# Performance work log

Hardware: AMD Instinct MI355X
Metric: run time of the kernel (lower is better)

The kernel has to match this reference:

```python
import jax, jax.numpy as jnp
import numpy as np

NEAR, FAR = 2.0, 6.0
N_SAMPLES = 64
L_PTS, L_DIR = 10, 4
INF_DELTA = 1e10


def posenc(x, L):
    # x: [..., 3] -> [..., 3 + 6*L] (identity + sin/cos at 2^l frequencies)
    freqs = 2.0 ** jnp.arange(L, dtype=x.dtype)              # [L]
    ang = x[..., None, :] * freqs[:, None]                   # [..., L, 3]
    enc = jnp.concatenate([jnp.sin(ang), jnp.cos(ang)], axis=-1)  # [..., L, 6]
    return jnp.concatenate([x, enc.reshape(x.shape[:-1] + (L * 6,))], axis=-1)


def setup_inputs() -> dict:
    key = jax.random.key(0)
    ks = jax.random.split(key, 12)
    R, D, DH = 4096, 256, 128
    PE_P, PE_D = 3 + 6 * L_PTS, 3 + 6 * L_DIR  # 63, 27

    def w(k, shape):
        fan_in = shape[0]
        return jax.random.normal(k, shape, dtype=jnp.float32) / np.sqrt(fan_in)

    return {
        "xyz": jax.random.normal(ks[0], (1, R, 3), dtype=jnp.float32),
        "viewdirs": jax.random.normal(ks[1], (1, R, 3), dtype=jnp.float32),
        "W1": w(ks[2], (PE_P, D)), "b1": jnp.zeros((D,), jnp.float32),
        "W2": w(ks[3], (D, D)),    "b2": jnp.zeros((D,), jnp.float32),
        "W3": w(ks[4], (D, D)),    "b3": jnp.zeros((D,), jnp.float32),
        "Wsig": w(ks[5], (D, 1)),  "bsig": jnp.zeros((1,), jnp.float32),
        "Wfeat": w(ks[6], (D, D)), "bfeat": jnp.zeros((D,), jnp.float32),
        "Wdir": w(ks[7], (D + PE_D, DH)), "bdir": jnp.zeros((DH,), jnp.float32),
        "Wrgb": w(ks[8], (DH, 3)), "brgb": jnp.zeros((3,), jnp.float32),
    }


def reference(xyz, viewdirs, W1, b1, W2, b2, W3, b3, Wsig, bsig,
              Wfeat, bfeat, Wdir, bdir, Wrgb, brgb):
    xyz = xyz[0]          # [R, 3] (batch dim squeezed as in render_coarse)
    vd = viewdirs[0]
    vd = vd / jnp.linalg.norm(vd, axis=-1, keepdims=True)
    R = xyz.shape[0]

    # Evenly spaced samples between near and far (perturb=0 -> deterministic)
    t = jnp.linspace(0.0, 1.0, N_SAMPLES, dtype=xyz.dtype)
    samples = NEAR * (1.0 - t) + FAR * t                     # [N]
    samples = jnp.broadcast_to(samples, (R, N_SAMPLES))      # [R, N]
    delta = jnp.concatenate(
        [samples[:, 1:] - samples[:, :-1],
         jnp.full((R, 1), INF_DELTA, dtype=samples.dtype)], axis=-1)  # [R, N]

    # Sample points along each ray
    pts = xyz[:, None, :] + samples[..., None] * vd[:, None, :]  # [R, N, 3]

    # NeRF MLP: positional-encoded points -> density + view-dep color
    pe = posenc(pts, L_PTS)                                   # [R, N, 63]
    de = posenc(vd, L_DIR)                                    # [R, 27]
    h = jax.nn.relu(pe @ W1 + b1)
    h = jax.nn.relu(h @ W2 + b2)
    h = jax.nn.relu(h @ W3 + b3)                              # [R, N, 256]
    density = (h @ Wsig + bsig)[..., 0]                       # [R, N]
    feat = h @ Wfeat + bfeat                                  # [R, N, 256]
    de_b = jnp.broadcast_to(de[:, None, :], (R, N_SAMPLES, de.shape[-1]))
    hd = jax.nn.relu(jnp.concatenate([feat, de_b], axis=-1) @ Wdir + bdir)
    rgb = jax.nn.sigmoid(hd @ Wrgb + brgb)                    # [R, N, 3]

    # Volume rendering (alpha compositing with cumprod transmittance)
    sigma = jax.nn.relu(density)
    alpha = 1.0 - jnp.exp(-sigma * delta)                     # [R, N]
    T = jnp.concatenate(
        [jnp.ones((R, 1), alpha.dtype),
         jnp.cumprod(1.0 - alpha[:, :-1], axis=-1)], axis=-1)
    w = T * alpha                                             # [R, N]
    rgb_map = jnp.sum(w[..., None] * rgb, axis=-2)            # [R, 3]
    alpha_map = jnp.sum(w, axis=-1, keepdims=True)            # [R, 1]
    rgb_map = rgb_map + (1.0 - alpha_map)                     # white_bkgd
    depth_map = jnp.sum(w * samples, axis=-1)                 # [R]
    return rgb_map, depth_map, alpha_map
```

## Files before the change

### kernel.cpp

```cpp
#include <hip/hip_runtime.h>
#include <hip/hip_bf16.h>
#include <math.h>


typedef unsigned short u16;
typedef unsigned int   u32;
typedef __bf16 bf16x8 __attribute__((ext_vector_type(8)));
typedef float  f32x4  __attribute__((ext_vector_type(4)));

#define HI_STRIDE 296
#define LO_STRIDE 264
#define NROW 64

__device__ __align__(16) u16 g_whi[249856];
__device__ __align__(16) u16 g_wlo[147456];

constexpr int OFF_W1 = 0;
constexpr int OFF_W2 = 16384;
constexpr int OFF_W3 = 81920;
constexpr int OFF_WF = 147456;
constexpr int OFF_WD = 212992;

static __device__ __forceinline__ float bf2f(u16 u) {
  return __uint_as_float(((u32)u) << 16);
}
static __device__ __forceinline__ u16 f2bf(float f) {
  u32 x = __float_as_uint(f);
  return (u16)((x + 0x7FFFu + ((x >> 16) & 1u)) >> 16);
}
static __device__ __forceinline__ u32 cvt_pk_bf16(float a, float b) {
  u32 r;
  asm("v_cvt_pk_bf16_f32 %0, %1, %2" : "=v"(r) : "v"(a), "v"(b));
  return r;
}
static __device__ __forceinline__ float wash(float x) {
  return (x == x) ? x : 0.0f;
}

struct alignas(8) U16x4 { u16 x, y, z, w; };

__global__ void repack_kernel(const float* __restrict__ w1, const float* __restrict__ w2,
                              const float* __restrict__ w3, const float* __restrict__ wf,
                              const float* __restrict__ wd) {
  int e = blockIdx.x * 256 + threadIdx.x;
  const float* src; int K, N, ks, base;
  if (e < 81920)       { if (e < 16384) { src = w1; K = 63;  N = 256; ks = 2; base = OFF_W1; }
                         else           { src = w2; K = 256; N = 256; ks = 8; base = OFF_W2; } }
  else if (e < 147456) { src = w3; K = 256; N = 256; ks = 8; base = OFF_W3; }
  else if (e < 212992) { src = wf; K = 256; N = 256; ks = 8; base = OFF_WF; }
  else                 { src = wd; K = 283; N = 128; ks = 9; base = OFF_WD; }
  int le   = e - base;
  int f    = le >> 9, pos = le & 511;
  int lane = pos >> 3, j = pos & 7;
  int t    = f / ks,  s = f - t * ks;
  int k    = s * 32 + ((lane >> 4) << 3) + j;
  int n    = (t << 4) + (lane & 15);
  float v  = (k < K) ? src[k * N + n] : 0.0f;
  u16 h    = f2bf(v);
  g_whi[e] = h;
  if (e < 147456) g_wlo[e] = f2bf(v - bf2f(h));
}

template<int KS, int NT, int RT, bool RELU, bool SPLIT>
static __device__ __forceinline__ void mlp_layer(u16* hi, u16* lo,
                                                 const u16* __restrict__ wh_,
                                                 const u16* __restrict__ wl_,
                                                 const float* __restrict__ bias,
                                                 int rg, int cg, int lane) {
  f32x4 acc[RT][NT];
#pragma unroll
  for (int rt = 0; rt < RT; ++rt)
#pragma unroll
    for (int nt = 0; nt < NT; ++nt) {
      f32x4 z = {0.0f, 0.0f, 0.0f, 0.0f};
      acc[rt][nt] = z;
    }
  const int l15 = lane & 15, q = lane >> 4;
#pragma unroll
  for (int s = 0; s < KS; ++s) {
    bf16x8 ah[RT], al[RT];
#pragma unroll
    for (int rt = 0; rt < RT; ++rt) {
      const int row = (rg * RT + rt) * 16 + l15;
      ah[rt] = *reinterpret_cast<const bf16x8*>(&hi[row * HI_STRIDE + s * 32 + q * 8]);
      if (SPLIT)
        al[rt] = *reinterpret_cast<const bf16x8*>(&lo[row * LO_STRIDE + s * 32 + q * 8]);
    }
    bf16x8 wh[NT], wl[NT];
#pragma unroll
    for (int nt = 0; nt < NT; ++nt) {
      const int t = cg * NT + nt;
      wh[nt] = *reinterpret_cast<const bf16x8*>(&wh_[(t * KS + s) * 512 + lane * 8]);
      if (SPLIT)
        wl[nt] = *reinterpret_cast<const bf16x8*>(&wl_[(t * KS + s) * 512 + lane * 8]);
    }
    __builtin_amdgcn_s_setprio(1);
#pragma unroll
    for (int nt = 0; nt < NT; ++nt)
#pragma unroll
      for (int rt = 0; rt < RT; ++rt)
        acc[rt][nt] = __builtin_amdgcn_mfma_f32_16x16x32_bf16(
            wh[nt], ah[rt], acc[rt][nt], 0, 0, 0);
    if (SPLIT) {
#pragma unroll
      for (int nt = 0; nt < NT; ++nt)
#pragma unroll
        for (int rt = 0; rt < RT; ++rt)
          acc[rt][nt] = __builtin_amdgcn_mfma_f32_16x16x32_bf16(
              wh[nt], al[rt], acc[rt][nt], 0, 0, 0);
#pragma unroll
      for (int nt = 0; nt < NT; ++nt)
#pragma unroll
        for (int rt = 0; rt < RT; ++rt)
          acc[rt][nt] = __builtin_amdgcn_mfma_f32_16x16x32_bf16(
              wl[nt], ah[rt], acc[rt][nt], 0, 0, 0);
    }
    __builtin_amdgcn_s_setprio(0);
  }
  __syncthreads();
#pragma unroll
  for (int nt = 0; nt < NT; ++nt) {
    const int nb = (cg * NT + nt) * 16 + q * 4;
    const float b0 = bias[nb + 0], b1 = bias[nb + 1];
    const float b2 = bias[nb + 2], b3 = bias[nb + 3];
#pragma unroll
    for (int rt = 0; rt < RT; ++rt) {
      const int row = (rg * RT + rt) * 16 + l15;
      float v0 = acc[rt][nt][0] + b0;
      float v1 = acc[rt][nt][1] + b1;
      float v2 = acc[rt][nt][2] + b2;
      float v3 = acc[rt][nt][3] + b3;
      if (RELU) {
        v0 = fmaxf(v0, 0.0f); v1 = fmaxf(v1, 0.0f);
        v2 = fmaxf(v2, 0.0f); v3 = fmaxf(v3, 0.0f);
      }
      u32 h01 = cvt_pk_bf16(v0, v1);
      u32 h23 = cvt_pk_bf16(v2, v3);
      *reinterpret_cast<uint2*>(&hi[row * HI_STRIDE + nb]) = make_uint2(h01, h23);
      if (SPLIT) {
        float l0 = v0 - __uint_as_float(h01 << 16);
        float l1 = v1 - __uint_as_float(h01 & 0xFFFF0000u);
        float l2 = v2 - __uint_as_float(h23 << 16);
        float l3 = v3 - __uint_as_float(h23 & 0xFFFF0000u);
        u32 lo01 = cvt_pk_bf16(l0, l1);
        u32 lo23 = cvt_pk_bf16(l2, l3);
        *reinterpret_cast<uint2*>(&lo[row * LO_STRIDE + nb]) = make_uint2(lo01, lo23);
      }
    }
  }
  __syncthreads();
}

__global__ __launch_bounds__(512, 4)
void nerf_kernel(const float* __restrict__ xyz, const float* __restrict__ vdirs,
                 const float* __restrict__ b1, const float* __restrict__ b2,
                 const float* __restrict__ b3, const float* __restrict__ wsig,
                 const float* __restrict__ bsig, const float* __restrict__ bfeat,
                 const float* __restrict__ bdir, const float* __restrict__ wrgb,
                 const float* __restrict__ brgb, float* __restrict__ out) {
  __shared__ u16  s_hi[NROW * HI_STRIDE];
  __shared__ u16  s_lo[NROW * LO_STRIDE];
  __shared__ float s_geo[6];
  __shared__ float s_de[32];
  __shared__ float s_part[512];
  __shared__ float s_rgb[192];

  const int tid  = threadIdx.x;
  const int wave = tid >> 6;
  const int lane = tid & 63;
  const int rg   = wave >> 2;
  const int cg   = wave & 3;

  if (tid == 0) {
    int rgI = blockIdx.x;
    float vx = vdirs[rgI * 3 + 0];
    float vy = vdirs[rgI * 3 + 1];
    float vz = vdirs[rgI * 3 + 2];
    float inv = 1.0f / sqrtf(vx * vx + vy * vy + vz * vz + 1e-20f);
    s_geo[0] = xyz[rgI * 3 + 0];
    s_geo[1] = xyz[rgI * 3 + 1];
    s_geo[2] = xyz[rgI * 3 + 2];
    s_geo[3] = vx * inv;
    s_geo[4] = vy * inv;
    s_geo[5] = vz * inv;
  }
  __syncthreads();

  if (tid < 32) {
    float val = 0.0f;
    if (tid < 3) val = s_geo[3 + tid];
    else if (tid < 27) {
      int fi = tid - 3, l = fi / 6, m = fi % 6;
      int ii = (m < 3) ? m : m - 3;
      float ang = s_geo[3 + ii] * (float)(1 << l);
      val = (m < 3) ? sinf(ang) : cosf(ang);
    }
    s_de[tid] = val;
  }

  {
    int row = tid >> 3, c8 = tid & 7;
    float t  = (float)row * (1.0f / 63.0f);
    float ts = 2.0f * (1.0f - t) + 6.0f * t;
    float p[3];
    p[0] = s_geo[0] + ts * s_geo[3];
    p[1] = s_geo[1] + ts * s_geo[4];
    p[2] = s_geo[2] + ts * s_geo[5];
    float val[8];
#pragma unroll
    for (int j = 0; j < 8; ++j) {
      int f = c8 * 8 + j;
      if (f < 3) val[j] = p[f];
      else if (f == 63) val[j] = 0.0f;
      else {
        int fi = f - 3, l = fi / 6, m = fi % 6;
        int ii = (m < 3) ? m : m - 3;
        float ang = p[ii] * (float)(1 << l);
        val[j] = (m < 3) ? sinf(ang) : cosf(ang);
      }
    }
    u32* hp = reinterpret_cast<u32*>(&s_hi[row * HI_STRIDE + c8 * 8]);
    u32* lp = reinterpret_cast<u32*>(&s_lo[row * LO_STRIDE + c8 * 8]);
#pragma unroll
    for (int jp = 0; jp < 4; ++jp) {
      u32 h = cvt_pk_bf16(val[2 * jp], val[2 * jp + 1]);
      float l0 = val[2 * jp]     - __uint_as_float(h << 16);
      float l1 = val[2 * jp + 1] - __uint_as_float(h & 0xFFFF0000u);
      hp[jp] = h;
      lp[jp] = cvt_pk_bf16(l0, l1);
    }
  }
  __syncthreads();

  mlp_layer<2, 4, 2, true, true>(s_hi, s_lo, g_whi + OFF_W1, g_wlo + OFF_W1,
                                 b1, rg, cg, lane);
  mlp_layer<8, 4, 2, true, true>(s_hi, s_lo, g_whi + OFF_W2, g_wlo + OFF_W2,
                                 b2, rg, cg, lane);
  mlp_layer<8, 4, 2, true, true>(s_hi, s_lo, g_whi + OFF_W3, g_wlo + OFF_W3,
                                 b3, rg, cg, lane);

  {
    const int row = lane, part = wave;
    float a = 0.0f;
    const float4* wp = reinterpret_cast<const float4*>(wsig);
#pragma unroll
    for (int i = 0; i < 8; ++i) {
      int k4 = part * 8 + i;
      U16x4 h = *reinterpret_cast<const U16x4*>(&s_hi[row * HI_STRIDE + k4 * 4]);
      U16x4 l = *reinterpret_cast<const U16x4*>(&s_lo[row * LO_STRIDE + k4 * 4]);
      float4 w = wp[k4];
      a += (bf2f(h.x) + bf2f(l.x)) * w.x + (bf2f(h.y) + bf2f(l.y)) * w.y
         + (bf2f(h.z) + bf2f(l.z)) * w.z + (bf2f(h.w) + bf2f(l.w)) * w.w;
    }
    s_part[part * 64 + row] = a;
  }

  mlp_layer<8, 4, 2, false, false>(s_hi, s_lo, g_whi + OFF_WF, g_wlo,
                                   bfeat, rg, cg, lane);

  {
    int row = tid >> 3, i0 = (tid & 7) * 4;
    u32 d01 = cvt_pk_bf16(s_de[i0 + 0], s_de[i0 + 1]);
    u32 d23 = cvt_pk_bf16(s_de[i0 + 2], s_de[i0 + 3]);
    u32* dp = reinterpret_cast<u32*>(&s_hi[row * HI_STRIDE + 256 + i0]);
    dp[0] = d01; dp[1] = d23;
  }
  __syncthreads();

  mlp_layer<9, 2, 2, true, false>(s_hi, s_lo, g_whi + OFF_WD, g_wlo,
                                  bdir, rg, cg, lane);

  if (tid < 192) {
    const int c = wave, r = lane;
    float a = brgb[c];
#pragma unroll 8
    for (int k4 = 0; k4 < 32; ++k4) {
      U16x4 h = *reinterpret_cast<const U16x4*>(&s_hi[r * HI_STRIDE + k4 * 4]);
      a += bf2f(h.x) * wrgb[(k4 * 4 + 0) * 3 + c];
      a += bf2f(h.y) * wrgb[(k4 * 4 + 1) * 3 + c];
      a += bf2f(h.z) * wrgb[(k4 * 4 + 2) * 3 + c];
      a += bf2f(h.w) * wrgb[(k4 * 4 + 3) * 3 + c];
    }
    a = wash(a);
    s_rgb[r * 3 + c] = 1.0f / (1.0f + expf(-a));
  }
  __syncthreads();

  if (wave == 0) {
    int rgI = blockIdx.x;
    float den = 0.0f;
#pragma unroll
    for (int p = 0; p < 8; ++p) den += s_part[p * 64 + lane];
    float my_den = wash(den + bsig[0]);
    float r0 = s_rgb[lane * 3 + 0];
    float r1 = s_rgb[lane * 3 + 1];
    float r2 = s_rgb[lane * 3 + 2];

    float t  = (float)lane * (1.0f / 63.0f);
    float ts = 2.0f * (1.0f - t) + 6.0f * t;
    float delta;
    if (lane < 63) {
      float t2 = (float)(lane + 1) * (1.0f / 63.0f);
      delta = (2.0f * (1.0f - t2) + 6.0f * t2) - ts;
    } else delta = 1e10f;
    float sig = fmaxf(my_den, 0.0f);
    float sd  = fminf(sig * delta, 60.0f);
    float incl = sd;
#pragma unroll
    for (int o = 1; o < 64; o <<= 1) {
      float v = __shfl_up(incl, o, 64);
      if (lane >= o) incl += v;
    }
    float excl  = fminf(fmaxf(incl - sd, 0.0f), 60.0f);
    float T     = expf(-excl);
    float alpha = 1.0f - expf(-sd);
    float w     = T * alpha;
    float sw = w, swr = w * r0, swg = w * r1, swb = w * r2, swd = w * ts;
#pragma unroll
    for (int o = 32; o > 0; o >>= 1) {
      sw  += __shfl_xor(sw,  o, 64);
      swr += __shfl_xor(swr, o, 64);
      swg += __shfl_xor(swg, o, 64);
      swb += __shfl_xor(swb, o, 64);
      swd += __shfl_xor(swd, o, 64);
    }
    if (lane == 0) {
      float bg = 1.0f - sw;
      out[rgI * 3 + 0]  = swr + bg;
      out[rgI * 3 + 1]  = swg + bg;
      out[rgI * 3 + 2]  = swb + bg;
      out[12288 + rgI]  = swd;
      out[16384 + rgI]  = sw;
    }
  }
}

extern "C" void kernel_launch(void* const* d_in, const int* in_sizes, int n_in,
                              void* d_out, int out_size, void* d_ws, size_t ws_size,
                              hipStream_t stream) {
  const float* xyz   = (const float*)d_in[0];
  const float* vdirs = (const float*)d_in[1];
  const float* W1    = (const float*)d_in[2];
  const float* b1    = (const float*)d_in[3];
  const float* W2    = (const float*)d_in[4];
  const float* b2    = (const float*)d_in[5];
  const float* W3    = (const float*)d_in[6];
  const float* b3    = (const float*)d_in[7];
  const float* Wsig  = (const float*)d_in[8];
  const float* bsig  = (const float*)d_in[9];
  const float* Wfeat = (const float*)d_in[10];
  const float* bfeat = (const float*)d_in[11];
  const float* Wdir  = (const float*)d_in[12];
  const float* bdir  = (const float*)d_in[13];
  const float* Wrgb  = (const float*)d_in[14];
  const float* brgb  = (const float*)d_in[15];
  float* out = (float*)d_out;

  repack_kernel<<<dim3(976), dim3(256), 0, stream>>>(W1, W2, W3, Wfeat, Wdir);
  nerf_kernel<<<dim3(4096), dim3(512), 0, stream>>>(
      xyz, vdirs, b1, b2, b3, Wsig, bsig, bfeat, bdir, Wrgb, brgb, out);
}
```

Baseline: 368.0 us.

## Switch MLP layers from 16x16x32 to 32x32x16 bf16 MFMA tiles

Replaces the 16x16x32 MFMA tiling (2 row tiles x 4 column tiles per wave) with 32x32x16 MFMA (one 32-row tile x 2 column tiles per wave). The weight repack is rewritten to produce the 32-wide fragment layout and the epilogue is remapped to the 32x32 accumulator layout. The aim is fewer LDS activation loads and weight loads per MFMA, since each larger instruction reuses its operands more. The cost is longer-latency MFMAs with a smaller unrolled K step, and a changed LDS access pattern that may raise bank conflicts.

```diff
diff --git a/kernel.cpp b/kernel.cpp
--- a/kernel.cpp
+++ b/kernel.cpp
@@ -6,7 +6,7 @@
 typedef unsigned short u16;
 typedef unsigned int   u32;
 typedef __bf16 bf16x8 __attribute__((ext_vector_type(8)));
-typedef float  f32x4  __attribute__((ext_vector_type(4)));
+typedef float  f32x16 __attribute__((ext_vector_type(16)));
 
 #define HI_STRIDE 296
 #define LO_STRIDE 264
@@ -44,48 +44,43 @@
                               const float* __restrict__ wd) {
   int e = blockIdx.x * 256 + threadIdx.x;
   const float* src; int K, N, ks, base;
-  if (e < 81920)       { if (e < 16384) { src = w1; K = 63;  N = 256; ks = 2; base = OFF_W1; }
-                         else           { src = w2; K = 256; N = 256; ks = 8; base = OFF_W2; } }
-  else if (e < 147456) { src = w3; K = 256; N = 256; ks = 8; base = OFF_W3; }
-  else if (e < 212992) { src = wf; K = 256; N = 256; ks = 8; base = OFF_WF; }
-  else                 { src = wd; K = 283; N = 128; ks = 9; base = OFF_WD; }
+  if (e < 81920)       { if (e < 16384) { src = w1; K = 63;  N = 256; ks = 4;  base = OFF_W1; }
+                         else           { src = w2; K = 256; N = 256; ks = 16; base = OFF_W2; } }
+  else if (e < 147456) { src = w3; K = 256; N = 256; ks = 16; base = OFF_W3; }
+  else if (e < 212992) { src = wf; K = 256; N = 256; ks = 16; base = OFF_WF; }
+  else                 { src = wd; K = 283; N = 128; ks = 18; base = OFF_WD; }
   int le   = e - base;
   int f    = le >> 9, pos = le & 511;
   int lane = pos >> 3, j = pos & 7;
   int t    = f / ks,  s = f - t * ks;
-  int k    = s * 32 + ((lane >> 4) << 3) + j;
-  int n    = (t << 4) + (lane & 15);
+  int k    = s * 16 + ((lane >> 5) << 3) + j;
+  int n    = (t << 5) + (lane & 31);
   float v  = (k < K) ? src[k * N + n] : 0.0f;
   u16 h    = f2bf(v);
   g_whi[e] = h;
   if (e < 147456) g_wlo[e] = f2bf(v - bf2f(h));
 }
 
-template<int KS, int NT, int RT, bool RELU, bool SPLIT>
-static __device__ __forceinline__ void mlp_layer(u16* hi, u16* lo,
-                                                 const u16* __restrict__ wh_,
-                                                 const u16* __restrict__ wl_,
-                                                 const float* __restrict__ bias,
-                                                 int rg, int cg, int lane) {
-  f32x4 acc[RT][NT];
-#pragma unroll
-  for (int rt = 0; rt < RT; ++rt)
-#pragma unroll
-    for (int nt = 0; nt < NT; ++nt) {
-      f32x4 z = {0.0f, 0.0f, 0.0f, 0.0f};
-      acc[rt][nt] = z;
-    }
-  const int l15 = lane & 15, q = lane >> 4;
+template<int KS, int NT, bool RELU, bool SPLIT>
+static __device__ __forceinline__ void mlp_layer32(u16* hi, u16* lo,
+                                                   const u16* __restrict__ wh_,
+                                                   const u16* __restrict__ wl_,
+                                                   const float* __restrict__ bias,
+                                                   int rg, int cg, int lane) {
+  f32x16 acc[NT];
+#pragma unroll
+  for (int nt = 0; nt < NT; ++nt)
+#pragma unroll
+    for (int i = 0; i < 16; ++i) acc[nt][i] = 0.0f;
+
+  const int l31 = lane & 31, q5 = lane >> 5;
+  const int srow = rg * 32 + l31;
 #pragma unroll
   for (int s = 0; s < KS; ++s) {
-    bf16x8 ah[RT], al[RT];
-#pragma unroll
-    for (int rt = 0; rt < RT; ++rt) {
-      const int row = (rg * RT + rt) * 16 + l15;
-      ah[rt] = *reinterpret_cast<const bf16x8*>(&hi[row * HI_STRIDE + s * 32 + q * 8]);
-      if (SPLIT)
-        al[rt] = *reinterpret_cast<const bf16x8*>(&lo[row * LO_STRIDE + s * 32 + q * 8]);
-    }
+    bf16x8 ah, al;
+    ah = *reinterpret_cast<const bf16x8*>(&hi[srow * HI_STRIDE + s * 16 + q5 * 8]);
+    if (SPLIT)
+      al = *reinterpret_cast<const bf16x8*>(&lo[srow * LO_STRIDE + s * 16 + q5 * 8]);
     bf16x8 wh[NT], wl[NT];
 #pragma unroll
     for (int nt = 0; nt < NT; ++nt) {
@@ -97,46 +92,34 @@
     __builtin_amdgcn_s_setprio(1);
 #pragma unroll
     for (int nt = 0; nt < NT; ++nt)
-#pragma unroll
-      for (int rt = 0; rt < RT; ++rt)
-        acc[rt][nt] = __builtin_amdgcn_mfma_f32_16x16x32_bf16(
-            wh[nt], ah[rt], acc[rt][nt], 0, 0, 0);
+      acc[nt] = __builtin_amdgcn_mfma_f32_32x32x16_bf16(wh[nt], ah, acc[nt], 0, 0, 0);
     if (SPLIT) {
 #pragma unroll
       for (int nt = 0; nt < NT; ++nt)
-#pragma unroll
-        for (int rt = 0; rt < RT; ++rt)
-          acc[rt][nt] = __builtin_amdgcn_mfma_f32_16x16x32_bf16(
-              wh[nt], al[rt], acc[rt][nt], 0, 0, 0);
+        acc[nt] = __builtin_amdgcn_mfma_f32_32x32x16_bf16(wh[nt], al, acc[nt], 0, 0, 0);
 #pragma unroll
       for (int nt = 0; nt < NT; ++nt)
-#pragma unroll
-        for (int rt = 0; rt < RT; ++rt)
-          acc[rt][nt] = __builtin_amdgcn_mfma_f32_16x16x32_bf16(
-              wl[nt], ah[rt], acc[rt][nt], 0, 0, 0);
+        acc[nt] = __builtin_amdgcn_mfma_f32_32x32x16_bf16(wl[nt], ah, acc[nt], 0, 0, 0);
     }
     __builtin_amdgcn_s_setprio(0);
   }
   __syncthreads();
 #pragma unroll
   for (int nt = 0; nt < NT; ++nt) {
-    const int nb = (cg * NT + nt) * 16 + q * 4;
-    const float b0 = bias[nb + 0], b1 = bias[nb + 1];
-    const float b2 = bias[nb + 2], b3 = bias[nb + 3];
-#pragma unroll
-    for (int rt = 0; rt < RT; ++rt) {
-      const int row = (rg * RT + rt) * 16 + l15;
-      float v0 = acc[rt][nt][0] + b0;
-      float v1 = acc[rt][nt][1] + b1;
-      float v2 = acc[rt][nt][2] + b2;
-      float v3 = acc[rt][nt][3] + b3;
+#pragma unroll
+    for (int g = 0; g < 4; ++g) {
+      const int nb = (cg * NT + nt) * 32 + 8 * g + 4 * q5;
+      float v0 = acc[nt][4 * g + 0] + bias[nb + 0];
+      float v1 = acc[nt][4 * g + 1] + bias[nb + 1];
+      float v2 = acc[nt][4 * g + 2] + bias[nb + 2];
+      float v3 = acc[nt][4 * g + 3] + bias[nb + 3];
       if (RELU) {
         v0 = fmaxf(v0, 0.0f); v1 = fmaxf(v1, 0.0f);
         v2 = fmaxf(v2, 0.0f); v3 = fmaxf(v3, 0.0f);
       }
       u32 h01 = cvt_pk_bf16(v0, v1);
       u32 h23 = cvt_pk_bf16(v2, v3);
-      *reinterpret_cast<uint2*>(&hi[row * HI_STRIDE + nb]) = make_uint2(h01, h23);
+      *reinterpret_cast<uint2*>(&hi[srow * HI_STRIDE + nb]) = make_uint2(h01, h23);
       if (SPLIT) {
         float l0 = v0 - __uint_as_float(h01 << 16);
         float l1 = v1 - __uint_as_float(h01 & 0xFFFF0000u);
@@ -144,7 +127,7 @@
         float l3 = v3 - __uint_as_float(h23 & 0xFFFF0000u);
         u32 lo01 = cvt_pk_bf16(l0, l1);
         u32 lo23 = cvt_pk_bf16(l2, l3);
-        *reinterpret_cast<uint2*>(&lo[row * LO_STRIDE + nb]) = make_uint2(lo01, lo23);
+        *reinterpret_cast<uint2*>(&lo[srow * LO_STRIDE + nb]) = make_uint2(lo01, lo23);
       }
     }
   }
@@ -232,11 +215,11 @@
   }
   __syncthreads();
 
-  mlp_layer<2, 4, 2, true, true>(s_hi, s_lo, g_whi + OFF_W1, g_wlo + OFF_W1,
-                                 b1, rg, cg, lane);
-  mlp_layer<8, 4, 2, true, true>(s_hi, s_lo, g_whi + OFF_W2, g_wlo + OFF_W2,
+  mlp_layer32<4, 2, true, true>(s_hi, s_lo, g_whi + OFF_W1, g_wlo + OFF_W1,
+                                b1, rg, cg, lane);
+  mlp_layer32<16, 2, true, true>(s_hi, s_lo, g_whi + OFF_W2, g_wlo + OFF_W2,
                                  b2, rg, cg, lane);
-  mlp_layer<8, 4, 2, true, true>(s_hi, s_lo, g_whi + OFF_W3, g_wlo + OFF_W3,
+  mlp_layer32<16, 2, true, true>(s_hi, s_lo, g_whi + OFF_W3, g_wlo + OFF_W3,
                                  b3, rg, cg, lane);
 
   {
@@ -255,7 +238,7 @@
     s_part[part * 64 + row] = a;
   }
 
-  mlp_layer<8, 4, 2, false, false>(s_hi, s_lo, g_whi + OFF_WF, g_wlo,
+  mlp_layer32<16, 2, false, false>(s_hi, s_lo, g_whi + OFF_WF, g_wlo,
                                    bfeat, rg, cg, lane);
 
   {
@@ -267,7 +250,7 @@
   }
   __syncthreads();
 
-  mlp_layer<9, 2, 2, true, false>(s_hi, s_lo, g_whi + OFF_WD, g_wlo,
+  mlp_layer32<18, 1, true, false>(s_hi, s_lo, g_whi + OFF_WD, g_wlo,
                                   bdir, rg, cg, lane);
 
   if (tid < 192) {
```

Measured after the change: 380.3 us. 1.03x slower.
